# Performance work log

Hardware: AMD Instinct MI355X
Metric: run time of the kernel (lower is better)

Reference implementation:

```python
import jax, jax.numpy as jnp
import numpy as np

E = 1024
H = 16
D = E // H  # 64
S = 2048
B = 4


def setup_inputs() -> dict:
    key = jax.random.key(0)
    ks = jax.random.split(key, 9)
    scale = 1.0 / np.sqrt(E)
    inp = {"x": jax.random.normal(ks[0], (S, B, E), dtype=jnp.float32)}
    for i, name in enumerate(["q", "k", "v", "o"]):
        inp[f"W{name}"] = jax.random.uniform(ks[1 + 2 * i], (E, E), dtype=jnp.float32, minval=-scale, maxval=scale)
        inp[f"b{name}"] = jax.random.uniform(ks[2 + 2 * i], (E,), dtype=jnp.float32, minval=-scale, maxval=scale)
    return inp


def reference(x, Wq, bq, Wk, bk, Wv, bv, Wo, bo):
    s, b, e = x.shape
    # linear projections (torch Linear: x @ W.T + b), split into heads
    q = (x @ Wq.T + bq).reshape(s, b, H, D)
    k = (x @ Wk.T + bk).reshape(s, b, H, D)
    v = (x @ Wv.T + bv).reshape(s, b, H, D)
    # naive O(S^2) attention, scores: [S, B, H, S]
    scores = jnp.einsum('sbhd,tbhd->sbht', q, k) / np.sqrt(D).astype(np.float32)
    attn = jax.nn.softmax(scores, axis=3)
    # dropout p=0.0 (eval) -> identity
    out = jnp.einsum('sbht,tbhd->sbhd', attn, v).reshape(s, b, e)
    return out @ Wo.T + bo
```

## Files before the change

kernel.cpp:

```cpp
#include <hip/hip_runtime.h>
#include <hip/hip_bf16.h>

#define S_LEN 2048
#define BATCH 4
#define EMB   1024
#define NH    16
#define HD    64
#define NROW  8192

#define QSCALE 0.18033688011112043f

typedef __bf16 bf16x8 __attribute__((ext_vector_type(8)));
typedef float  f32x4  __attribute__((ext_vector_type(4)));

typedef __attribute__((address_space(3))) void lds_void;
typedef const __attribute__((address_space(1))) void gbl_void;
#define GLOAD_LDS16(g, l) __builtin_amdgcn_global_load_lds((gbl_void*)(g), (lds_void*)(l), 16, 0, 0)
#define MFMA16(a, b, c) __builtin_amdgcn_mfma_f32_16x16x32_bf16((a), (b), (c), 0, 0, 0)

#if __has_builtin(__builtin_amdgcn_exp2f)
#define EXP2(x) __builtin_amdgcn_exp2f(x)
#else
#define EXP2(x) __expf((x) * 0.6931471805599453f)
#endif

__global__ void cvt_bf16_kernel(const float* __restrict__ src,
                                __bf16* __restrict__ dst, int n4) {
    int i = blockIdx.x * blockDim.x + threadIdx.x;
    if (i >= n4) return;
    float4 v = ((const float4*)src)[i];
    union { __bf16 h[4]; short4 s4; } u;
    u.h[0] = (__bf16)v.x; u.h[1] = (__bf16)v.y;
    u.h[2] = (__bf16)v.z; u.h[3] = (__bf16)v.w;
    ((short4*)dst)[i] = u.s4;
}

__global__ __launch_bounds__(256) void gemm_qkv_kernel(
    const __bf16* __restrict__ A,
    const __bf16* __restrict__ W0, const __bf16* __restrict__ W1,
    const __bf16* __restrict__ W2,
    const float* __restrict__ bi0, const float* __restrict__ bi1,
    const float* __restrict__ bi2,
    __bf16* __restrict__ Qo, __bf16* __restrict__ Ko, __bf16* __restrict__ Vo)
{
    __shared__ __bf16 As[128 * 32];
    __shared__ __bf16 Bs[128 * 32];
    const int gid = blockIdx.x;
    const int mB = gid / 24, nB = gid % 24;
    const int which = nB >> 3;
    const __bf16* W = which == 0 ? W0 : (which == 1 ? W1 : W2);
    const float* bias = which == 0 ? bi0 : (which == 1 ? bi1 : bi2);
    __bf16* outb = which == 0 ? Qo : (which == 1 ? Ko : Vo);
    const int m0 = mB * 128;
    const int n0 = (nB & 7) * 128;

    const int lane = threadIdx.x & 63;
    const int wave = threadIdx.x >> 6;
    const int l15 = lane & 15;
    const int quad = lane >> 4;
    const int wm = (wave >> 1) * 64;
    const int wn = (wave & 1) * 64;

    const int c0 = wave * 128 + lane;
    const int c1 = c0 + 64;
    const int ar0 = c0 >> 2, ak0 = (c0 & 3) * 8;
    const int ar1 = c1 >> 2, ak1 = (c1 & 3) * 8;

    const __bf16* Ag = A + (size_t)m0 * EMB;
    const __bf16* Wg = W + (size_t)n0 * EMB;

    f32x4 acc[4][4];
#pragma unroll
    for (int i = 0; i < 4; ++i)
#pragma unroll
        for (int j = 0; j < 4; ++j) acc[i][j] = (f32x4){0.f, 0.f, 0.f, 0.f};

    for (int k0 = 0; k0 < EMB; k0 += 32) {
        __syncthreads();
        GLOAD_LDS16(Ag + (size_t)ar0 * EMB + k0 + ak0, As + wave * 1024);
        GLOAD_LDS16(Ag + (size_t)ar1 * EMB + k0 + ak1, As + wave * 1024 + 512);
        GLOAD_LDS16(Wg + (size_t)ar0 * EMB + k0 + ak0, Bs + wave * 1024);
        GLOAD_LDS16(Wg + (size_t)ar1 * EMB + k0 + ak1, Bs + wave * 1024 + 512);
        __syncthreads();

        bf16x8 af[4], bf[4];
#pragma unroll
        for (int t = 0; t < 4; ++t) {
            af[t] = *(const bf16x8*)(As + (wm + t * 16 + l15) * 32 + quad * 8);
            bf[t] = *(const bf16x8*)(Bs + (wn + t * 16 + l15) * 32 + quad * 8);
        }
#pragma unroll
        for (int i = 0; i < 4; ++i)
#pragma unroll
            for (int j = 0; j < 4; ++j)
                acc[i][j] = MFMA16(af[i], bf[j], acc[i][j]);
    }

#pragma unroll
    for (int j = 0; j < 4; ++j) {
        const int col = n0 + wn + j * 16 + l15;
        const float bv = bias[col];
        const int h = col >> 6, d = col & 63;
#pragma unroll
        for (int i = 0; i < 4; ++i) {
#pragma unroll
            for (int r = 0; r < 4; ++r) {
                const int m = m0 + wm + i * 16 + quad * 4 + r;
                float v = acc[i][j][r] + bv;
                if (which == 0) v *= QSCALE;
                const int b = m & 3, s = m >> 2;
                if (which == 2)
                    outb[((size_t)(b * NH + h) * HD + d) * S_LEN + s] = (__bf16)v;
                else
                    outb[((size_t)(b * NH + h) * S_LEN + s) * HD + d] = (__bf16)v;
            }
        }
    }
}

__global__ __launch_bounds__(256) void gemm_out_kernel(
    const __bf16* __restrict__ A, const __bf16* __restrict__ W,
    const float* __restrict__ bias, float* __restrict__ outf)
{
    __shared__ __bf16 As[128 * 32];
    __shared__ __bf16 Bs[128 * 32];
    const int lane = threadIdx.x & 63;
    const int wave = threadIdx.x >> 6;
    const int m0 = (blockIdx.x >> 3) * 128;
    const int n0 = (blockIdx.x & 7) * 128;
    const int l15 = lane & 15;
    const int quad = lane >> 4;
    const int wm = (wave >> 1) * 64;
    const int wn = (wave & 1) * 64;

    const int c0 = wave * 128 + lane;
    const int c1 = c0 + 64;
    const int ar0 = c0 >> 2, ak0 = (c0 & 3) * 8;
    const int ar1 = c1 >> 2, ak1 = (c1 & 3) * 8;

    const __bf16* Ag = A + (size_t)m0 * EMB;
    const __bf16* Wg = W + (size_t)n0 * EMB;

    f32x4 acc[4][4];
#pragma unroll
    for (int i = 0; i < 4; ++i)
#pragma unroll
        for (int j = 0; j < 4; ++j) acc[i][j] = (f32x4){0.f, 0.f, 0.f, 0.f};

    for (int k0 = 0; k0 < EMB; k0 += 32) {
        __syncthreads();
        GLOAD_LDS16(Ag + (size_t)ar0 * EMB + k0 + ak0, As + wave * 1024);
        GLOAD_LDS16(Ag + (size_t)ar1 * EMB + k0 + ak1, As + wave * 1024 + 512);
        GLOAD_LDS16(Wg + (size_t)ar0 * EMB + k0 + ak0, Bs + wave * 1024);
        GLOAD_LDS16(Wg + (size_t)ar1 * EMB + k0 + ak1, Bs + wave * 1024 + 512);
        __syncthreads();

        bf16x8 af[4], bf[4];
#pragma unroll
        for (int t = 0; t < 4; ++t) {
            af[t] = *(const bf16x8*)(As + (wm + t * 16 + l15) * 32 + quad * 8);
            bf[t] = *(const bf16x8*)(Bs + (wn + t * 16 + l15) * 32 + quad * 8);
        }
#pragma unroll
        for (int i = 0; i < 4; ++i)
#pragma unroll
            for (int j = 0; j < 4; ++j)
                acc[i][j] = MFMA16(af[i], bf[j], acc[i][j]);
    }

#pragma unroll
    for (int j = 0; j < 4; ++j) {
        const int col = n0 + wn + j * 16 + l15;
        const float bv = bias[col];
#pragma unroll
        for (int i = 0; i < 4; ++i)
#pragma unroll
            for (int r = 0; r < 4; ++r) {
                const int m = m0 + wm + i * 16 + quad * 4 + r;
                outf[(size_t)m * EMB + col] = acc[i][j][r] + bv;
            }
    }
}

__global__ __launch_bounds__(256, 4) void attn_kernel(
    const __bf16* __restrict__ Q, const __bf16* __restrict__ Kp,
    const __bf16* __restrict__ Vt, __bf16* __restrict__ Ao)
{
    __shared__ __align__(16) __bf16 Ks[2][32 * 64];
    __shared__ __align__(16) __bf16 Vs[2][32 * 64];
    __shared__ __align__(16) __bf16 Ps[4][32 * 40];

    const int tid = threadIdx.x;
    const int lane = tid & 63;
    const int wave = tid >> 6;
    const int l15 = lane & 15;
    const int quad = lane >> 4;
    const int bh = blockIdx.y;
    const int b = bh >> 4, h = bh & 15;
    const int qw = blockIdx.x * 128 + wave * 32;

    const __bf16* Qb = Q  + (size_t)bh * S_LEN * HD;
    const __bf16* Kb = Kp + (size_t)bh * S_LEN * HD;
    const __bf16* Vb = Vt + (size_t)bh * HD * S_LEN;

    const int kr = tid >> 3;
    const int ks = (((tid & 7) ^ ((tid >> 4) & 7))) * 8;
    const int vr = tid >> 2;
    const int vs = (((tid & 3) ^ ((tid >> 3) & 3))) * 8;

    bf16x8 qf[2][2];
#pragma unroll
    for (int mi = 0; mi < 2; ++mi)
#pragma unroll
        for (int kc = 0; kc < 2; ++kc)
            qf[mi][kc] = *(const bf16x8*)(Qb + (size_t)(qw + mi * 16 + l15) * HD
                                          + kc * 32 + quad * 8);

    bf16x8 ones;
#pragma unroll
    for (int i = 0; i < 8; ++i) ones[i] = (__bf16)1.0f;

    f32x4 acco[2][4], accl[2];
#pragma unroll
    for (int mi = 0; mi < 2; ++mi) {
        accl[mi] = (f32x4){0.f, 0.f, 0.f, 0.f};
#pragma unroll
        for (int nt = 0; nt < 4; ++nt) acco[mi][nt] = (f32x4){0.f, 0.f, 0.f, 0.f};
    }

    GLOAD_LDS16(Kb + (size_t)kr * HD + ks, &Ks[0][wave * 512]);
    GLOAD_LDS16(Vb + (size_t)vr * S_LEN + vs, &Vs[0][wave * 512]);

    for (int it = 0; it < S_LEN / 32; ++it) {
        const int bi = it & 1;
        __syncthreads();
        if (it + 1 < S_LEN / 32) {
            const int t0 = (it + 1) * 32;
            GLOAD_LDS16(Kb + (size_t)(t0 + kr) * HD + ks, &Ks[bi ^ 1][wave * 512]);
            GLOAD_LDS16(Vb + (size_t)vr * S_LEN + t0 + vs, &Vs[bi ^ 1][wave * 512]);
        }
        const __bf16* Kt = &Ks[bi][0];
        const __bf16* Vl = &Vs[bi][0];
        __bf16* Pw = &Ps[wave][0];

        bf16x8 kf[2][2];
#pragma unroll
        for (int p = 0; p < 2; ++p) {
            const int r = 2 * l15 + p;
            const int x = l15 & 7;
#pragma unroll
            for (int kc = 0; kc < 2; ++kc)
                kf[p][kc] = *(const bf16x8*)(Kt + r * 64 + (((kc * 4 + quad) ^ x) << 3));
        }
#pragma unroll
        for (int mi = 0; mi < 2; ++mi) {
            f32x4 se = {0.f, 0.f, 0.f, 0.f}, so = {0.f, 0.f, 0.f, 0.f};
            se = MFMA16(qf[mi][0], kf[0][0], se);
            se = MFMA16(qf[mi][1], kf[0][1], se);
            so = MFMA16(qf[mi][0], kf[1][0], so);
            so = MFMA16(qf[mi][1], kf[1][1], so);
#pragma unroll
            for (int r = 0; r < 4; ++r) {
                float pe = EXP2(se[r]);
                float po = EXP2(so[r]);
                union { __bf16 hh[2]; unsigned u; } pk;
                pk.hh[0] = (__bf16)pe;
                pk.hh[1] = (__bf16)po;
                *(unsigned*)(Pw + (mi * 16 + quad * 4 + r) * 40 + 2 * l15) = pk.u;
            }
        }
        bf16x8 pf[2];
#pragma unroll
        for (int mi = 0; mi < 2; ++mi) {
            pf[mi] = *(const bf16x8*)(Pw + (mi * 16 + l15) * 40 + quad * 8);
            accl[mi] = MFMA16(pf[mi], ones, accl[mi]);
        }
#pragma unroll
        for (int nt = 0; nt < 4; ++nt) {
            const int rv = nt * 16 + l15;
            const int xv = (l15 >> 1) & 3;
            bf16x8 vf = *(const bf16x8*)(Vl + rv * 32 + (((quad ^ xv)) << 3));
#pragma unroll
            for (int mi = 0; mi < 2; ++mi)
                acco[mi][nt] = MFMA16(pf[mi], vf, acco[mi][nt]);
        }
    }

#pragma unroll
    for (int mi = 0; mi < 2; ++mi)
#pragma unroll
        for (int r = 0; r < 4; ++r) {
            const float inv = 1.0f / accl[mi][r];
            const int srow = qw + mi * 16 + quad * 4 + r;
            const int n = srow * BATCH + b;
#pragma unroll
            for (int nt = 0; nt < 4; ++nt)
                Ao[(size_t)n * EMB + h * 64 + nt * 16 + l15] =
                    (__bf16)(acco[mi][nt][r] * inv);
        }
}

extern "C" void kernel_launch(void* const* d_in, const int* in_sizes, int n_in,
                              void* d_out, int out_size, void* d_ws, size_t ws_size,
                              hipStream_t stream) {
    const float* x  = (const float*)d_in[0];
    const float* Wq = (const float*)d_in[1];
    const float* bq = (const float*)d_in[2];
    const float* Wk = (const float*)d_in[3];
    const float* bk = (const float*)d_in[4];
    const float* Wv = (const float*)d_in[5];
    const float* bv = (const float*)d_in[6];
    const float* Wo = (const float*)d_in[7];
    const float* bo = (const float*)d_in[8];
    float* out = (float*)d_out;

    char* ws = (char*)d_ws;
    const size_t xbf_sz = (size_t)NROW * EMB * 2;
    const size_t wbf_sz = (size_t)EMB * EMB * 2;
    const size_t qkv_sz = (size_t)BATCH * NH * S_LEN * HD * 2;
    __bf16* x_bf  = (__bf16*)ws;  ws += xbf_sz;
    __bf16* Wq_bf = (__bf16*)ws;  ws += wbf_sz;
    __bf16* Wk_bf = (__bf16*)ws;  ws += wbf_sz;
    __bf16* Wv_bf = (__bf16*)ws;  ws += wbf_sz;
    __bf16* Wo_bf = (__bf16*)ws;  ws += wbf_sz;
    __bf16* Qb    = (__bf16*)ws;  ws += qkv_sz;
    __bf16* Kb    = (__bf16*)ws;  ws += qkv_sz;
    __bf16* Vtb   = (__bf16*)ws;  ws += qkv_sz;
    __bf16* Aob   = (__bf16*)ws;  ws += qkv_sz;

    {
        int n4 = NROW * EMB / 4;
        cvt_bf16_kernel<<<(n4 + 255) / 256, 256, 0, stream>>>(x, x_bf, n4);
        int w4 = EMB * EMB / 4;
        cvt_bf16_kernel<<<(w4 + 255) / 256, 256, 0, stream>>>(Wq, Wq_bf, w4);
        cvt_bf16_kernel<<<(w4 + 255) / 256, 256, 0, stream>>>(Wk, Wk_bf, w4);
        cvt_bf16_kernel<<<(w4 + 255) / 256, 256, 0, stream>>>(Wv, Wv_bf, w4);
        cvt_bf16_kernel<<<(w4 + 255) / 256, 256, 0, stream>>>(Wo, Wo_bf, w4);
    }
    gemm_qkv_kernel<<<64 * 24, 256, 0, stream>>>(x_bf, Wq_bf, Wk_bf, Wv_bf,
                                                 bq, bk, bv, Qb, Kb, Vtb);
    dim3 ag(S_LEN / 128, BATCH * NH);
    attn_kernel<<<ag, 256, 0, stream>>>(Qb, Kb, Vtb, Aob);
    gemm_out_kernel<<<(NROW / 128) * (EMB / 128), 256, 0, stream>>>(Aob, Wo_bf, bo, out);
}
```

Baseline: 310.4 us.

## Triple-buffer GEMM and attention loads, swizzle LDS, remap blocks per XCD, fuse conversions

The GEMM and attention main loops move from single or double buffering to a three-stage LDS ring, and explicit vmcnt waits plus one barrier per step replace the two __syncthreads. GEMM tiles get an XOR swizzle on LDS columns to cut bank conflicts. Block indices are remapped so that blocks sharing an M-tile or a head land on the same XCD, improving L2 reuse. The five conversion launches are merged into one kernel. LDS use grows, which may lower occupancy, and the hand-written waitcnt counts must match the number of loads actually in flight.

```diff
diff --git a/kernel.cpp b/kernel.cpp
--- a/kernel.cpp
+++ b/kernel.cpp
@@ -24,10 +24,24 @@
 #define EXP2(x) __expf((x) * 0.6931471805599453f)
 #endif
 
-__global__ void cvt_bf16_kernel(const float* __restrict__ src,
-                                __bf16* __restrict__ dst, int n4) {
-    int i = blockIdx.x * blockDim.x + threadIdx.x;
-    if (i >= n4) return;
+__global__ void cvt_all_kernel(const float* __restrict__ x,
+                               const float* __restrict__ wq, const float* __restrict__ wk,
+                               const float* __restrict__ wv, const float* __restrict__ wo,
+                               __bf16* __restrict__ xb,
+                               __bf16* __restrict__ qb, __bf16* __restrict__ kb,
+                               __bf16* __restrict__ vb, __bf16* __restrict__ ob) {
+    const int bid = blockIdx.x;
+    const float* src;
+    __bf16* dst;
+    int i;
+    if (bid < 8192) {
+        src = x; dst = xb; i = bid * 256 + threadIdx.x;
+    } else {
+        const int w = (bid - 8192) >> 10;
+        src = w == 0 ? wq : (w == 1 ? wk : (w == 2 ? wv : wo));
+        dst = w == 0 ? qb : (w == 1 ? kb : (w == 2 ? vb : ob));
+        i = ((bid - 8192) & 1023) * 256 + threadIdx.x;
+    }
     float4 v = ((const float4*)src)[i];
     union { __bf16 h[4]; short4 s4; } u;
     u.h[0] = (__bf16)v.x; u.h[1] = (__bf16)v.y;
@@ -43,10 +57,12 @@
     const float* __restrict__ bi2,
     __bf16* __restrict__ Qo, __bf16* __restrict__ Ko, __bf16* __restrict__ Vo)
 {
-    __shared__ __bf16 As[128 * 32];
-    __shared__ __bf16 Bs[128 * 32];
-    const int gid = blockIdx.x;
-    const int mB = gid / 24, nB = gid % 24;
+    __shared__ __bf16 As[3][128 * 32];
+    __shared__ __bf16 Bs[3][128 * 32];
+    const int flat = blockIdx.x;
+    const int xcd = flat & 7, slot = flat >> 3;
+    const int nB = slot >> 3;
+    const int mB = (xcd << 3) | (slot & 7);
     const int which = nB >> 3;
     const __bf16* W = which == 0 ? W0 : (which == 1 ? W1 : W2);
     const float* bias = which == 0 ? bi0 : (which == 1 ? bi1 : bi2);
@@ -63,8 +79,8 @@
 
     const int c0 = wave * 128 + lane;
     const int c1 = c0 + 64;
-    const int ar0 = c0 >> 2, ak0 = (c0 & 3) * 8;
-    const int ar1 = c1 >> 2, ak1 = (c1 & 3) * 8;
+    const int ar0 = c0 >> 2, ak0 = (((c0 & 3) ^ ((c0 >> 3) & 3))) * 8;
+    const int ar1 = c1 >> 2, ak1 = (((c1 & 3) ^ ((c1 >> 3) & 3))) * 8;
 
     const __bf16* Ag = A + (size_t)m0 * EMB;
     const __bf16* Wg = W + (size_t)n0 * EMB;
@@ -75,25 +91,38 @@
 #pragma unroll
         for (int j = 0; j < 4; ++j) acc[i][j] = (f32x4){0.f, 0.f, 0.f, 0.f};
 
-    for (int k0 = 0; k0 < EMB; k0 += 32) {
-        __syncthreads();
-        GLOAD_LDS16(Ag + (size_t)ar0 * EMB + k0 + ak0, As + wave * 1024);
-        GLOAD_LDS16(Ag + (size_t)ar1 * EMB + k0 + ak1, As + wave * 1024 + 512);
-        GLOAD_LDS16(Wg + (size_t)ar0 * EMB + k0 + ak0, Bs + wave * 1024);
-        GLOAD_LDS16(Wg + (size_t)ar1 * EMB + k0 + ak1, Bs + wave * 1024 + 512);
-        __syncthreads();
-
-        bf16x8 af[4], bf[4];
-#pragma unroll
-        for (int t = 0; t < 4; ++t) {
-            af[t] = *(const bf16x8*)(As + (wm + t * 16 + l15) * 32 + quad * 8);
-            bf[t] = *(const bf16x8*)(Bs + (wn + t * 16 + l15) * 32 + quad * 8);
+    auto stage = [&](int t, int buf) {
+        const int kk = t * 32;
+        GLOAD_LDS16(Ag + (size_t)ar0 * EMB + kk + ak0, &As[buf][wave * 1024]);
+        GLOAD_LDS16(Ag + (size_t)ar1 * EMB + kk + ak1, &As[buf][wave * 1024 + 512]);
+        GLOAD_LDS16(Wg + (size_t)ar0 * EMB + kk + ak0, &Bs[buf][wave * 1024]);
+        GLOAD_LDS16(Wg + (size_t)ar1 * EMB + kk + ak1, &Bs[buf][wave * 1024 + 512]);
+    };
+    stage(0, 0);
+    stage(1, 1);
+
+    const int xr = (l15 >> 1) & 3;
+    int bt = 0;
+    for (int t = 0; t < 32; ++t) {
+        if (t < 31) asm volatile("s_waitcnt vmcnt(4)" ::: "memory");
+        else        asm volatile("s_waitcnt vmcnt(0)" ::: "memory");
+        __builtin_amdgcn_s_barrier();
+        if (t + 2 < 32) {
+            int wb = bt + 2; if (wb >= 3) wb -= 3;
+            stage(t + 2, wb);
+        }
+        bf16x8 af[4], bfr[4];
+#pragma unroll
+        for (int tt = 0; tt < 4; ++tt) {
+            af[tt]  = *(const bf16x8*)(&As[bt][0] + (wm + tt * 16 + l15) * 32 + ((quad ^ xr) << 3));
+            bfr[tt] = *(const bf16x8*)(&Bs[bt][0] + (wn + tt * 16 + l15) * 32 + ((quad ^ xr) << 3));
         }
 #pragma unroll
         for (int i = 0; i < 4; ++i)
 #pragma unroll
             for (int j = 0; j < 4; ++j)
-                acc[i][j] = MFMA16(af[i], bf[j], acc[i][j]);
+                acc[i][j] = MFMA16(af[i], bfr[j], acc[i][j]);
+        if (++bt == 3) bt = 0;
     }
 
 #pragma unroll
@@ -122,12 +151,17 @@
     const __bf16* __restrict__ A, const __bf16* __restrict__ W,
     const float* __restrict__ bias, float* __restrict__ outf)
 {
-    __shared__ __bf16 As[128 * 32];
-    __shared__ __bf16 Bs[128 * 32];
+    __shared__ __bf16 As[3][128 * 32];
+    __shared__ __bf16 Bs[3][128 * 32];
+    const int flat = blockIdx.x;
+    const int xcd = flat & 7, slot = flat >> 3;
+    const int nB = slot >> 3;
+    const int mB = (xcd << 3) | (slot & 7);
+    const int m0 = mB * 128;
+    const int n0 = nB * 128;
+
     const int lane = threadIdx.x & 63;
     const int wave = threadIdx.x >> 6;
-    const int m0 = (blockIdx.x >> 3) * 128;
-    const int n0 = (blockIdx.x & 7) * 128;
     const int l15 = lane & 15;
     const int quad = lane >> 4;
     const int wm = (wave >> 1) * 64;
@@ -135,8 +169,8 @@
 
     const int c0 = wave * 128 + lane;
     const int c1 = c0 + 64;
-    const int ar0 = c0 >> 2, ak0 = (c0 & 3) * 8;
-    const int ar1 = c1 >> 2, ak1 = (c1 & 3) * 8;
+    const int ar0 = c0 >> 2, ak0 = (((c0 & 3) ^ ((c0 >> 3) & 3))) * 8;
+    const int ar1 = c1 >> 2, ak1 = (((c1 & 3) ^ ((c1 >> 3) & 3))) * 8;
 
     const __bf16* Ag = A + (size_t)m0 * EMB;
     const __bf16* Wg = W + (size_t)n0 * EMB;
@@ -147,25 +181,38 @@
 #pragma unroll
         for (int j = 0; j < 4; ++j) acc[i][j] = (f32x4){0.f, 0.f, 0.f, 0.f};
 
-    for (int k0 = 0; k0 < EMB; k0 += 32) {
-        __syncthreads();
-        GLOAD_LDS16(Ag + (size_t)ar0 * EMB + k0 + ak0, As + wave * 1024);
-        GLOAD_LDS16(Ag + (size_t)ar1 * EMB + k0 + ak1, As + wave * 1024 + 512);
-        GLOAD_LDS16(Wg + (size_t)ar0 * EMB + k0 + ak0, Bs + wave * 1024);
-        GLOAD_LDS16(Wg + (size_t)ar1 * EMB + k0 + ak1, Bs + wave * 1024 + 512);
-        __syncthreads();
-
-        bf16x8 af[4], bf[4];
-#pragma unroll
-        for (int t = 0; t < 4; ++t) {
-            af[t] = *(const bf16x8*)(As + (wm + t * 16 + l15) * 32 + quad * 8);
-            bf[t] = *(const bf16x8*)(Bs + (wn + t * 16 + l15) * 32 + quad * 8);
+    auto stage = [&](int t, int buf) {
+        const int kk = t * 32;
+        GLOAD_LDS16(Ag + (size_t)ar0 * EMB + kk + ak0, &As[buf][wave * 1024]);
+        GLOAD_LDS16(Ag + (size_t)ar1 * EMB + kk + ak1, &As[buf][wave * 1024 + 512]);
+        GLOAD_LDS16(Wg + (size_t)ar0 * EMB + kk + ak0, &Bs[buf][wave * 1024]);
+        GLOAD_LDS16(Wg + (size_t)ar1 * EMB + kk + ak1, &Bs[buf][wave * 1024 + 512]);
+    };
+    stage(0, 0);
+    stage(1, 1);
+
+    const int xr = (l15 >> 1) & 3;
+    int bt = 0;
+    for (int t = 0; t < 32; ++t) {
+        if (t < 31) asm volatile("s_waitcnt vmcnt(4)" ::: "memory");
+        else        asm volatile("s_waitcnt vmcnt(0)" ::: "memory");
+        __builtin_amdgcn_s_barrier();
+        if (t + 2 < 32) {
+            int wb = bt + 2; if (wb >= 3) wb -= 3;
+            stage(t + 2, wb);
+        }
+        bf16x8 af[4], bfr[4];
+#pragma unroll
+        for (int tt = 0; tt < 4; ++tt) {
+            af[tt]  = *(const bf16x8*)(&As[bt][0] + (wm + tt * 16 + l15) * 32 + ((quad ^ xr) << 3));
+            bfr[tt] = *(const bf16x8*)(&Bs[bt][0] + (wn + tt * 16 + l15) * 32 + ((quad ^ xr) << 3));
         }
 #pragma unroll
         for (int i = 0; i < 4; ++i)
 #pragma unroll
             for (int j = 0; j < 4; ++j)
-                acc[i][j] = MFMA16(af[i], bf[j], acc[i][j]);
+                acc[i][j] = MFMA16(af[i], bfr[j], acc[i][j]);
+        if (++bt == 3) bt = 0;
     }
 
 #pragma unroll
@@ -186,8 +233,8 @@
     const __bf16* __restrict__ Q, const __bf16* __restrict__ Kp,
     const __bf16* __restrict__ Vt, __bf16* __restrict__ Ao)
 {
-    __shared__ __align__(16) __bf16 Ks[2][32 * 64];
-    __shared__ __align__(16) __bf16 Vs[2][32 * 64];
+    __shared__ __align__(16) __bf16 Ks[3][32 * 64];
+    __shared__ __align__(16) __bf16 Vs[3][32 * 64];
     __shared__ __align__(16) __bf16 Ps[4][32 * 40];
 
     const int tid = threadIdx.x;
@@ -195,9 +242,12 @@
     const int wave = tid >> 6;
     const int l15 = lane & 15;
     const int quad = lane >> 4;
-    const int bh = blockIdx.y;
+
+    const int flat = blockIdx.y * gridDim.x + blockIdx.x;
+    const int nf = (flat & 7) * 128 + (flat >> 3);
+    const int bh = nf >> 4;
     const int b = bh >> 4, h = bh & 15;
-    const int qw = blockIdx.x * 128 + wave * 32;
+    const int qw = (nf & 15) * 128 + wave * 32;
 
     const __bf16* Qb = Q  + (size_t)bh * S_LEN * HD;
     const __bf16* Kb = Kp + (size_t)bh * S_LEN * HD;
@@ -228,19 +278,25 @@
         for (int nt = 0; nt < 4; ++nt) acco[mi][nt] = (f32x4){0.f, 0.f, 0.f, 0.f};
     }
 
-    GLOAD_LDS16(Kb + (size_t)kr * HD + ks, &Ks[0][wave * 512]);
-    GLOAD_LDS16(Vb + (size_t)vr * S_LEN + vs, &Vs[0][wave * 512]);
-
+    auto stageKV = [&](int t, int buf) {
+        const int t0 = t * 32;
+        GLOAD_LDS16(Kb + (size_t)(t0 + kr) * HD + ks, &Ks[buf][wave * 512]);
+        GLOAD_LDS16(Vb + (size_t)vr * S_LEN + t0 + vs, &Vs[buf][wave * 512]);
+    };
+    stageKV(0, 0);
+    stageKV(1, 1);
+
+    int bt = 0;
     for (int it = 0; it < S_LEN / 32; ++it) {
-        const int bi = it & 1;
-        __syncthreads();
-        if (it + 1 < S_LEN / 32) {
-            const int t0 = (it + 1) * 32;
-            GLOAD_LDS16(Kb + (size_t)(t0 + kr) * HD + ks, &Ks[bi ^ 1][wave * 512]);
-            GLOAD_LDS16(Vb + (size_t)vr * S_LEN + t0 + vs, &Vs[bi ^ 1][wave * 512]);
-        }
-        const __bf16* Kt = &Ks[bi][0];
-        const __bf16* Vl = &Vs[bi][0];
+        if (it < S_LEN / 32 - 1) asm volatile("s_waitcnt vmcnt(2)" ::: "memory");
+        else                     asm volatile("s_waitcnt vmcnt(0)" ::: "memory");
+        __builtin_amdgcn_s_barrier();
+        if (it + 2 < S_LEN / 32) {
+            int wb = bt + 2; if (wb >= 3) wb -= 3;
+            stageKV(it + 2, wb);
+        }
+        const __bf16* Kt = &Ks[bt][0];
+        const __bf16* Vl = &Vs[bt][0];
         __bf16* Pw = &Ps[wave][0];
 
         bf16x8 kf[2][2];
@@ -284,6 +340,7 @@
             for (int mi = 0; mi < 2; ++mi)
                 acco[mi][nt] = MFMA16(pf[mi], vf, acco[mi][nt]);
         }
+        if (++bt == 3) bt = 0;
     }
 
 #pragma unroll
@@ -328,15 +385,9 @@
     __bf16* Vtb   = (__bf16*)ws;  ws += qkv_sz;
     __bf16* Aob   = (__bf16*)ws;  ws += qkv_sz;
 
-    {
-        int n4 = NROW * EMB / 4;
-        cvt_bf16_kernel<<<(n4 + 255) / 256, 256, 0, stream>>>(x, x_bf, n4);
-        int w4 = EMB * EMB / 4;
-        cvt_bf16_kernel<<<(w4 + 255) / 256, 256, 0, stream>>>(Wq, Wq_bf, w4);
-        cvt_bf16_kernel<<<(w4 + 255) / 256, 256, 0, stream>>>(Wk, Wk_bf, w4);
-        cvt_bf16_kernel<<<(w4 + 255) / 256, 256, 0, stream>>>(Wv, Wv_bf, w4);
-        cvt_bf16_kernel<<<(w4 + 255) / 256, 256, 0, stream>>>(Wo, Wo_bf, w4);
-    }
+    cvt_all_kernel<<<8192 + 4 * 1024, 256, 0, stream>>>(
+        x, Wq, Wk, Wv, Wo, x_bf, Wq_bf, Wk_bf, Wv_bf, Wo_bf);
+
     gemm_qkv_kernel<<<64 * 24, 256, 0, stream>>>(x_bf, Wq_bf, Wk_bf, Wv_bf,
                                                  bq, bk, bv, Qb, Kb, Vtb);
     dim3 ag(S_LEN / 128, BATCH * NH);
```

After: 290.6 us. 1.07x faster.
